# Optimization experiments

Measured on AMD Instinct MI355X. Metric: run time of the kernel, lower is better.

Reference implementation:

```python
import jax, jax.numpy as jnp
import numpy as np

B, S, H = 4, 2048, 1024
NH, HD = 16, 64


def setup_inputs() -> dict:
    key = jax.random.key(0)
    ks = jax.random.split(key, 5)
    scale = 1.0 / np.sqrt(H)
    x = jax.random.normal(ks[0], (B, S, H), dtype=jnp.float32)
    w_qkv = jax.random.normal(ks[1], (H, 3 * H), dtype=jnp.float32) * scale
    b_qkv = jnp.zeros((3 * H,), dtype=jnp.float32)
    w_out = jax.random.normal(ks[2], (H, H), dtype=jnp.float32) * scale
    b_out = jnp.zeros((H,), dtype=jnp.float32)
    return {"x": x, "w_qkv": w_qkv, "b_qkv": b_qkv, "w_out": w_out, "b_out": b_out}


def reference(x, w_qkv, b_qkv, w_out, b_out):
    bsz, seq_len, hidden = x.shape
    qkv = x @ w_qkv + b_qkv  # [B,S,3H]
    q, k, v = jnp.split(qkv, 3, axis=-1)

    def heads(t):
        return t.reshape(bsz, seq_len, NH, HD).transpose(0, 2, 1, 3)  # [B,NH,S,HD]

    q, k, v = heads(q), heads(k), heads(v)
    scale = HD ** (-0.5)
    attn = jnp.einsum("bhqd,bhkd->bhqk", q, k) * scale  # [B,NH,S,S]
    causal = jnp.tril(jnp.ones((seq_len, seq_len), dtype=bool))
    attn = jnp.where(causal, attn, -jnp.inf)
    probs = jax.nn.softmax(attn, axis=-1)
    out = jnp.einsum("bhqk,bhkd->bhqd", probs, v)
    out = out.transpose(0, 2, 1, 3).reshape(bsz, seq_len, hidden)
    return out @ w_out + b_out
```

## Files before the change

kernel.cpp:

```cpp
#include <hip/hip_runtime.h>
#include <hip/hip_bf16.h>
#include <cstdint>

#define B_  4
#define S_  2048
#define H_  1024
#define NH_ 16
#define HD_ 64

using short8  = __attribute__((ext_vector_type(8))) short;
using floatx4 = __attribute__((ext_vector_type(4))) float;

__device__ __forceinline__ unsigned short f2b(float f) {
  union { float f; unsigned int u; } x; x.f = f;
  unsigned int r = x.u + 0x7fffu + ((x.u >> 16) & 1u);
  return (unsigned short)(r >> 16);
}
__device__ __forceinline__ unsigned short f2b_fast(float f) {
  union { float f; unsigned int u; } x; x.f = f;
  return (unsigned short)((x.u + 0x8000u) >> 16);
}
__device__ __forceinline__ unsigned int pack2(float a, float b) {
  return (unsigned int)f2b(a) | ((unsigned int)f2b(b) << 16);
}

__device__ __forceinline__ void async16(void* lds, const void* g) {
  __builtin_amdgcn_global_load_lds(
      (const __attribute__((address_space(1))) unsigned int*)g,
      (__attribute__((address_space(3))) unsigned int*)lds, 16, 0, 0);
}

__global__ void k_convert(const float* __restrict__ in, unsigned short* __restrict__ out, int n) {
  int i = (blockIdx.x * blockDim.x + threadIdx.x) * 4;
  if (i >= n) return;
  float4 v = *(const float4*)(in + i);
  ushort4 o;
  o.x = f2b(v.x); o.y = f2b(v.y); o.z = f2b(v.z); o.w = f2b(v.w);
  *(ushort4*)(out + i) = o;
}

__global__ void k_transpose_convert(const float* __restrict__ in, unsigned short* __restrict__ out,
                                    int R, int C) {
  __shared__ float tile[32][33];
  int tx = threadIdx.x & 31, ty = threadIdx.x >> 5;
  int c0 = blockIdx.x * 32, r0 = blockIdx.y * 32;
  for (int i = 0; i < 4; i++) {
    int r = r0 + ty + i * 8;
    tile[ty + i * 8][tx] = in[(size_t)r * C + c0 + tx];
  }
  __syncthreads();
  for (int i = 0; i < 4; i++) {
    int c = c0 + ty + i * 8;
    out[(size_t)c * R + r0 + tx] = f2b(tile[tx][ty + i * 8]);
  }
}

template <bool OUT_BF16>
__global__ __launch_bounds__(256, 3) void k_gemm_bt(
    const unsigned short* __restrict__ A,
    const unsigned short* __restrict__ BT,
    const float* __restrict__ bias,
    void* __restrict__ Cout,
    unsigned short* __restrict__ vt,
    int M, int N, int K) {
  __shared__ __align__(16) unsigned short As[2][128 * 32];
  __shared__ __align__(16) unsigned short Bs[2][128 * 32];
  const int tid  = threadIdx.x;
  const int lane = tid & 63, wave = tid >> 6;
  const int quad = lane >> 4, l16 = lane & 15;
  const int wm = wave >> 1, wn = wave & 1;
  const int m0 = blockIdx.y * 128, n0 = blockIdx.x * 128;
  const int wv2 = wave & 1;

  const unsigned short* srcbase = (wave < 2) ? A : BT;
  const int base0 = (wave < 2) ? m0 : n0;

  floatx4 acc[4][4];
  for (int mt = 0; mt < 4; mt++)
    for (int nt = 0; nt < 4; nt++)
      acc[mt][nt] = (floatx4){0.f, 0.f, 0.f, 0.f};

  auto stage = [&](int k0, int bufi) {
    unsigned short* dst = (wave < 2) ? &As[bufi][0] : &Bs[bufi][0];
    for (int j = 0; j < 4; j++) {
      int c = wv2 * 256 + j * 64 + lane;
      int row = c >> 2, slot = c & 3;
      int c8 = slot ^ ((row >> 1) & 3);
      async16(&dst[c * 8], &srcbase[(size_t)(base0 + row) * K + k0 + c8 * 8]);
    }
  };

  stage(0, 0);
  int it = 0;
  for (int k0 = 0; k0 < K; k0 += 32, it++) {
    const int cur = it & 1;
    __syncthreads();
    if (k0 + 32 < K) stage(k0 + 32, cur ^ 1);
    short8 af[4], bq[4];
    for (int t = 0; t < 4; t++) {
      int ra = wm * 64 + t * 16 + l16;
      int rb = wn * 64 + t * 16 + l16;
      af[t] = *(const short8*)&As[cur][(ra * 4 + (quad ^ ((ra >> 1) & 3))) * 8];
      bq[t] = *(const short8*)&Bs[cur][(rb * 4 + (quad ^ ((rb >> 1) & 3))) * 8];
    }
    for (int mt = 0; mt < 4; mt++)
      for (int nt = 0; nt < 4; nt++)
        acc[mt][nt] = __builtin_amdgcn_mfma_f32_16x16x32_bf16(af[mt], bq[nt], acc[mt][nt], 0, 0, 0);
  }

  if (OUT_BF16 && n0 >= 2048) {
    for (int mt = 0; mt < 4; mt++) {
      int row0 = m0 + wm * 64 + mt * 16 + quad * 4;
      int b = row0 >> 11, s = row0 & 2047;
      for (int nt = 0; nt < 4; nt++) {
        int col = n0 + wn * 64 + nt * 16 + l16;
        float bv = bias[col];
        uint2 u;
        u.x = pack2(acc[mt][nt][0] + bv, acc[mt][nt][1] + bv);
        u.y = pack2(acc[mt][nt][2] + bv, acc[mt][nt][3] + bv);
        *(uint2*)&vt[(size_t)(b * 1024 + (col - 2048)) * S_ + s] = u;
      }
    }
  } else {
    for (int mt = 0; mt < 4; mt++) {
      int row = m0 + wm * 64 + mt * 16 + quad * 4;
      for (int nt = 0; nt < 4; nt++) {
        int col = n0 + wn * 64 + nt * 16 + l16;
        float bv = bias[col];
        for (int r = 0; r < 4; r++) {
          float v = acc[mt][nt][r] + bv;
          if (OUT_BF16) ((unsigned short*)Cout)[(size_t)(row + r) * N + col] = f2b(v);
          else          ((float*)Cout)[(size_t)(row + r) * N + col] = v;
        }
      }
    }
  }
}

__global__ __launch_bounds__(256, 3) void k_attn(
    const unsigned short* __restrict__ qkv,
    const unsigned short* __restrict__ vt,
    unsigned short* __restrict__ outb) {
  __shared__ __align__(16) unsigned short Ks [2][64 * 64];
  __shared__ __align__(16) unsigned short VTs[2][64 * 64];
  __shared__ __align__(16) unsigned short Ps[4][2][16 * 64];

  const int tid  = threadIdx.x;
  const int lane = tid & 63, w = tid >> 6;
  const int quad = lane >> 4, l16 = lane & 15;
  const int qt = (S_ / 128 - 1) - (blockIdx.x >> 6);
  const int bh = blockIdx.x & 63;
  const int b = bh >> 4, h = bh & 15;
  const int qwv = qt * 128 + w * 32;
  const int wv2 = w & 1;

  short8 qf[2][2];
  for (int g = 0; g < 2; g++)
    for (int kh = 0; kh < 2; kh++)
      qf[g][kh] = *(const short8*)&qkv[(size_t)(b * S_ + qwv + g * 16 + l16) * (3 * H_)
                                       + h * HD_ + kh * 32 + quad * 8];

  floatx4 oacc[2][4];
  float lsum[2] = {0.f, 0.f};
  for (int g = 0; g < 2; g++)
    for (int ct = 0; ct < 4; ct++) oacc[g][ct] = (floatx4){0.f, 0.f, 0.f, 0.f};

  auto stage = [&](int kt, int bufi) {
    if (w < 2) {
      for (int j = 0; j < 4; j++) {
        int c = wv2 * 256 + j * 64 + lane;
        int row = c >> 3, c8 = (c & 7) ^ (row & 7);
        async16(&Ks[bufi][c * 8],
                &qkv[(size_t)(b * S_ + kt * 64 + row) * (3 * H_) + H_ + h * HD_ + c8 * 8]);
      }
    } else {
      for (int j = 0; j < 4; j++) {
        int c = wv2 * 256 + j * 64 + lane;
        int row = c >> 3, c8 = (c & 7) ^ (row & 7);
        async16(&VTs[bufi][c * 8],
                &vt[(size_t)(bh * HD_ + row) * S_ + kt * 64 + c8 * 8]);
      }
    }
  };

  const int ktmax = 2 * qt + 1;
  stage(0, 0);
  for (int kt = 0; kt <= ktmax; kt++) {
    const int cur = kt & 1;
    __syncthreads();
    if (kt < ktmax) stage(kt + 1, cur ^ 1);

    if (kt * 64 <= qwv + 31) {
      const bool need_mask = (kt * 64 + 63 > qwv);

      for (int ct = 0; ct < 4; ct++) {
        int krow = ct * 16 + l16;
        short8 kf0 = *(const short8*)&Ks[cur][(krow * 8 + ((0 + quad) ^ (krow & 7))) * 8];
        short8 kf1 = *(const short8*)&Ks[cur][(krow * 8 + ((4 + quad) ^ (krow & 7))) * 8];
        int slot = (ct * 2 + (quad >> 1)) ^ (l16 & 7);
        for (int g = 0; g < 2; g++) {
          floatx4 z = (floatx4){0.f, 0.f, 0.f, 0.f};
          z = __builtin_amdgcn_mfma_f32_16x16x32_bf16(kf0, qf[g][0], z, 0, 0, 0);
          z = __builtin_amdgcn_mfma_f32_16x16x32_bf16(kf1, qf[g][1], z, 0, 0, 0);
          float p[4];
          if (need_mask) {
            int kvb = kt * 64 + ct * 16 + quad * 4;
            int q = qwv + g * 16 + l16;
            for (int r = 0; r < 4; r++)
              p[r] = (kvb + r <= q) ? __expf(z[r] * 0.125f) : 0.f;
          } else {
            for (int r = 0; r < 4; r++) p[r] = __expf(z[r] * 0.125f);
          }
          lsum[g] += (p[0] + p[1]) + (p[2] + p[3]);
          uint2 u;
          u.x = (unsigned int)f2b_fast(p[0]) | ((unsigned int)f2b_fast(p[1]) << 16);
          u.y = (unsigned int)f2b_fast(p[2]) | ((unsigned int)f2b_fast(p[3]) << 16);
          *(uint2*)&Ps[w][g][l16 * 64 + slot * 8 + (quad & 1) * 4] = u;
        }
      }

      short8 vf[4][2];
      for (int ct = 0; ct < 4; ct++)
        for (int kh = 0; kh < 2; kh++) {
          int vrow = ct * 16 + l16;
          vf[ct][kh] = *(const short8*)&VTs[cur][(vrow * 8 + ((kh * 4 + quad) ^ (vrow & 7))) * 8];
        }

      for (int g = 0; g < 2; g++)
        for (int kh = 0; kh < 2; kh++) {
          short8 pf = *(const short8*)&Ps[w][g][l16 * 64 + ((kh * 4 + quad) ^ (l16 & 7)) * 8];
          for (int ct = 0; ct < 4; ct++)
            oacc[g][ct] = __builtin_amdgcn_mfma_f32_16x16x32_bf16(vf[ct][kh], pf, oacc[g][ct], 0, 0, 0);
        }
    }
  }

  for (int g = 0; g < 2; g++) {
    lsum[g] += __shfl_xor(lsum[g], 16);
    lsum[g] += __shfl_xor(lsum[g], 32);
  }

  for (int g = 0; g < 2; g++) {
    float inv = 1.0f / lsum[g];
    int q = qwv + g * 16 + l16;
    for (int ct = 0; ct < 4; ct++) {
      uint2 u;
      u.x = pack2(oacc[g][ct][0] * inv, oacc[g][ct][1] * inv);
      u.y = pack2(oacc[g][ct][2] * inv, oacc[g][ct][3] * inv);
      *(uint2*)&outb[(size_t)(b * S_ + q) * H_ + h * HD_ + ct * 16 + quad * 4] = u;
    }
  }
}

extern "C" void kernel_launch(void* const* d_in, const int* in_sizes, int n_in,
                              void* d_out, int out_size, void* d_ws, size_t ws_size,
                              hipStream_t stream) {
  const float* x     = (const float*)d_in[0];
  const float* w_qkv = (const float*)d_in[1];
  const float* b_qkv = (const float*)d_in[2];
  const float* w_out = (const float*)d_in[3];
  const float* b_out = (const float*)d_in[4];

  char* ws = (char*)d_ws;
  size_t off = 0;
  auto alloc = [&](size_t bytes) -> void* {
    void* p = ws + off;
    off = (off + bytes + 255) & ~(size_t)255;
    return p;
  };
  unsigned short* xb    = (unsigned short*)alloc((size_t)B_ * S_ * H_ * 2);
  unsigned short* wqkvT = (unsigned short*)alloc((size_t)3 * H_ * H_ * 2);
  unsigned short* woutT = (unsigned short*)alloc((size_t)H_ * H_ * 2);
  unsigned short* qkv   = (unsigned short*)alloc((size_t)B_ * S_ * 3 * H_ * 2);
  unsigned short* ao    = (unsigned short*)alloc((size_t)B_ * S_ * H_ * 2);
  unsigned short* vtb   = (unsigned short*)alloc((size_t)B_ * NH_ * HD_ * S_ * 2);

  const int nx = B_ * S_ * H_;
  k_convert<<<nx / 4 / 256, 256, 0, stream>>>(x, xb, nx);
  k_transpose_convert<<<dim3(3 * H_ / 32, H_ / 32), 256, 0, stream>>>(w_qkv, wqkvT, H_, 3 * H_);
  k_transpose_convert<<<dim3(H_ / 32, H_ / 32), 256, 0, stream>>>(w_out, woutT, H_, H_);

  k_gemm_bt<true ><<<dim3(3 * H_ / 128, B_ * S_ / 128), 256, 0, stream>>>(
      xb, wqkvT, b_qkv, qkv, vtb, B_ * S_, 3 * H_, H_);

  k_attn<<<(S_ / 128) * 64, 256, 0, stream>>>(qkv, vtb, ao);

  k_gemm_bt<false><<<dim3(H_ / 128, B_ * S_ / 128), 256, 0, stream>>>(
      ao, woutT, b_out, (float*)d_out, nullptr, B_ * S_, H_, H_);
}
```

Measured before the change: 250.9 us.

## Enlarge attention query tile to 256 rows and fuse prep kernels

The attention kernel now processes 256 query rows per block (64 per wave, four 16-row groups), so each K/V tile staged into LDS is reused across twice as many queries. The grid becomes 512 blocks with a paired ordering of query tiles meant to balance causal work, and per-group skip checks avoid fully masked tiles. Launch bounds drop to 2 blocks/CU to fit the larger accumulators. The three input conversion and transpose kernels are merged into one launch to cut launch overhead. The cost is more register pressure, lower occupancy and fewer blocks to spread across CUs.

```diff
diff --git a/kernel.cpp b/kernel.cpp
--- a/kernel.cpp
+++ b/kernel.cpp
@@ -30,20 +30,11 @@
       (__attribute__((address_space(3))) unsigned int*)lds, 16, 0, 0);
 }
 
-__global__ void k_convert(const float* __restrict__ in, unsigned short* __restrict__ out, int n) {
-  int i = (blockIdx.x * blockDim.x + threadIdx.x) * 4;
-  if (i >= n) return;
-  float4 v = *(const float4*)(in + i);
-  ushort4 o;
-  o.x = f2b(v.x); o.y = f2b(v.y); o.z = f2b(v.z); o.w = f2b(v.w);
-  *(ushort4*)(out + i) = o;
-}
-
-__global__ void k_transpose_convert(const float* __restrict__ in, unsigned short* __restrict__ out,
-                                    int R, int C) {
+__device__ __forceinline__ void transpose_tile(const float* __restrict__ in,
+                                               unsigned short* __restrict__ out,
+                                               int R, int C, int c0, int r0) {
   __shared__ float tile[32][33];
   int tx = threadIdx.x & 31, ty = threadIdx.x >> 5;
-  int c0 = blockIdx.x * 32, r0 = blockIdx.y * 32;
   for (int i = 0; i < 4; i++) {
     int r = r0 + ty + i * 8;
     tile[ty + i * 8][tx] = in[(size_t)r * C + c0 + tx];
@@ -52,6 +43,26 @@
   for (int i = 0; i < 4; i++) {
     int c = c0 + ty + i * 8;
     out[(size_t)c * R + r0 + tx] = f2b(tile[tx][ty + i * 8]);
+  }
+}
+
+__global__ void k_prep(const float* __restrict__ x, const float* __restrict__ w_qkv,
+                       const float* __restrict__ w_out,
+                       unsigned short* __restrict__ xb, unsigned short* __restrict__ wqkvT,
+                       unsigned short* __restrict__ woutT) {
+  int bx = blockIdx.x;
+  if (bx < 8192) {
+    int i = (bx * 256 + threadIdx.x) * 4;
+    float4 v = *(const float4*)(x + i);
+    ushort4 o;
+    o.x = f2b(v.x); o.y = f2b(v.y); o.z = f2b(v.z); o.w = f2b(v.w);
+    *(ushort4*)(xb + i) = o;
+  } else if (bx < 8192 + 3072) {
+    int t = bx - 8192;
+    transpose_tile(w_qkv, wqkvT, H_, 3 * H_, (t % 96) * 32, (t / 96) * 32);
+  } else {
+    int t = bx - 8192 - 3072;
+    transpose_tile(w_out, woutT, H_, H_, (t & 31) * 32, (t >> 5) * 32);
   }
 }
 
@@ -137,7 +148,7 @@
   }
 }
 
-__global__ __launch_bounds__(256, 3) void k_attn(
+__global__ __launch_bounds__(256, 2) void k_attn(
     const unsigned short* __restrict__ qkv,
     const unsigned short* __restrict__ vt,
     unsigned short* __restrict__ outb) {
@@ -148,21 +159,22 @@
   const int tid  = threadIdx.x;
   const int lane = tid & 63, w = tid >> 6;
   const int quad = lane >> 4, l16 = lane & 15;
-  const int qt = (S_ / 128 - 1) - (blockIdx.x >> 6);
-  const int bh = blockIdx.x & 63;
+  const int bx = blockIdx.x;
+  const int qt = (bx < 256) ? 7 - (bx >> 6) : (bx >> 6) - 4;
+  const int bh = bx & 63;
   const int b = bh >> 4, h = bh & 15;
-  const int qwv = qt * 128 + w * 32;
+  const int qwv = qt * 256 + w * 64;
   const int wv2 = w & 1;
 
-  short8 qf[2][2];
-  for (int g = 0; g < 2; g++)
+  short8 qf[4][2];
+  for (int g = 0; g < 4; g++)
     for (int kh = 0; kh < 2; kh++)
       qf[g][kh] = *(const short8*)&qkv[(size_t)(b * S_ + qwv + g * 16 + l16) * (3 * H_)
                                        + h * HD_ + kh * 32 + quad * 8];
 
-  floatx4 oacc[2][4];
-  float lsum[2] = {0.f, 0.f};
-  for (int g = 0; g < 2; g++)
+  floatx4 oacc[4][4];
+  float lsum[4] = {0.f, 0.f, 0.f, 0.f};
+  for (int g = 0; g < 4; g++)
     for (int ct = 0; ct < 4; ct++) oacc[g][ct] = (floatx4){0.f, 0.f, 0.f, 0.f};
 
   auto stage = [&](int kt, int bufi) {
@@ -183,41 +195,15 @@
     }
   };
 
-  const int ktmax = 2 * qt + 1;
+  const int ktmax = 4 * qt + 3;
   stage(0, 0);
   for (int kt = 0; kt <= ktmax; kt++) {
     const int cur = kt & 1;
     __syncthreads();
     if (kt < ktmax) stage(kt + 1, cur ^ 1);
 
-    if (kt * 64 <= qwv + 31) {
+    if (kt * 64 <= qwv + 63) {
       const bool need_mask = (kt * 64 + 63 > qwv);
-
-      for (int ct = 0; ct < 4; ct++) {
-        int krow = ct * 16 + l16;
-        short8 kf0 = *(const short8*)&Ks[cur][(krow * 8 + ((0 + quad) ^ (krow & 7))) * 8];
-        short8 kf1 = *(const short8*)&Ks[cur][(krow * 8 + ((4 + quad) ^ (krow & 7))) * 8];
-        int slot = (ct * 2 + (quad >> 1)) ^ (l16 & 7);
-        for (int g = 0; g < 2; g++) {
-          floatx4 z = (floatx4){0.f, 0.f, 0.f, 0.f};
-          z = __builtin_amdgcn_mfma_f32_16x16x32_bf16(kf0, qf[g][0], z, 0, 0, 0);
-          z = __builtin_amdgcn_mfma_f32_16x16x32_bf16(kf1, qf[g][1], z, 0, 0, 0);
-          float p[4];
-          if (need_mask) {
-            int kvb = kt * 64 + ct * 16 + quad * 4;
-            int q = qwv + g * 16 + l16;
-            for (int r = 0; r < 4; r++)
-              p[r] = (kvb + r <= q) ? __expf(z[r] * 0.125f) : 0.f;
-          } else {
-            for (int r = 0; r < 4; r++) p[r] = __expf(z[r] * 0.125f);
-          }
-          lsum[g] += (p[0] + p[1]) + (p[2] + p[3]);
-          uint2 u;
-          u.x = (unsigned int)f2b_fast(p[0]) | ((unsigned int)f2b_fast(p[1]) << 16);
-          u.y = (unsigned int)f2b_fast(p[2]) | ((unsigned int)f2b_fast(p[3]) << 16);
-          *(uint2*)&Ps[w][g][l16 * 64 + slot * 8 + (quad & 1) * 4] = u;
-        }
-      }
 
       short8 vf[4][2];
       for (int ct = 0; ct < 4; ct++)
@@ -226,21 +212,57 @@
           vf[ct][kh] = *(const short8*)&VTs[cur][(vrow * 8 + ((kh * 4 + quad) ^ (vrow & 7))) * 8];
         }
 
-      for (int g = 0; g < 2; g++)
-        for (int kh = 0; kh < 2; kh++) {
-          short8 pf = *(const short8*)&Ps[w][g][l16 * 64 + ((kh * 4 + quad) ^ (l16 & 7)) * 8];
-          for (int ct = 0; ct < 4; ct++)
-            oacc[g][ct] = __builtin_amdgcn_mfma_f32_16x16x32_bf16(vf[ct][kh], pf, oacc[g][ct], 0, 0, 0);
+      for (int gp = 0; gp < 2; gp++) {
+        const int g0 = gp * 2;
+        if (kt * 64 > qwv + (g0 + 1) * 16 + 15) continue;
+
+        for (int ct = 0; ct < 4; ct++) {
+          int krow = ct * 16 + l16;
+          short8 kf0 = *(const short8*)&Ks[cur][(krow * 8 + ((0 + quad) ^ (krow & 7))) * 8];
+          short8 kf1 = *(const short8*)&Ks[cur][(krow * 8 + ((4 + quad) ^ (krow & 7))) * 8];
+          int slot = (ct * 2 + (quad >> 1)) ^ (l16 & 7);
+          for (int gi = 0; gi < 2; gi++) {
+            int g = g0 + gi;
+            if (kt * 64 > qwv + g * 16 + 15) continue;
+            floatx4 z = (floatx4){0.f, 0.f, 0.f, 0.f};
+            z = __builtin_amdgcn_mfma_f32_16x16x32_bf16(kf0, qf[g][0], z, 0, 0, 0);
+            z = __builtin_amdgcn_mfma_f32_16x16x32_bf16(kf1, qf[g][1], z, 0, 0, 0);
+            float p[4];
+            if (need_mask) {
+              int kvb = kt * 64 + ct * 16 + quad * 4;
+              int q = qwv + g * 16 + l16;
+              for (int r = 0; r < 4; r++)
+                p[r] = (kvb + r <= q) ? __expf(z[r] * 0.125f) : 0.f;
+            } else {
+              for (int r = 0; r < 4; r++) p[r] = __expf(z[r] * 0.125f);
+            }
+            lsum[g] += (p[0] + p[1]) + (p[2] + p[3]);
+            uint2 u;
+            u.x = (unsigned int)f2b_fast(p[0]) | ((unsigned int)f2b_fast(p[1]) << 16);
+            u.y = (unsigned int)f2b_fast(p[2]) | ((unsigned int)f2b_fast(p[3]) << 16);
+            *(uint2*)&Ps[w][gi][l16 * 64 + slot * 8 + (quad & 1) * 4] = u;
+          }
         }
-    }
-  }
-
-  for (int g = 0; g < 2; g++) {
+
+        for (int gi = 0; gi < 2; gi++) {
+          int g = g0 + gi;
+          if (kt * 64 > qwv + g * 16 + 15) continue;
+          for (int kh = 0; kh < 2; kh++) {
+            short8 pf = *(const short8*)&Ps[w][gi][l16 * 64 + ((kh * 4 + quad) ^ (l16 & 7)) * 8];
+            for (int ct = 0; ct < 4; ct++)
+              oacc[g][ct] = __builtin_amdgcn_mfma_f32_16x16x32_bf16(vf[ct][kh], pf, oacc[g][ct], 0, 0, 0);
+          }
+        }
+      }
+    }
+  }
+
+  for (int g = 0; g < 4; g++) {
     lsum[g] += __shfl_xor(lsum[g], 16);
     lsum[g] += __shfl_xor(lsum[g], 32);
   }
 
-  for (int g = 0; g < 2; g++) {
+  for (int g = 0; g < 4; g++) {
     float inv = 1.0f / lsum[g];
     int q = qwv + g * 16 + l16;
     for (int ct = 0; ct < 4; ct++) {
@@ -275,15 +297,12 @@
   unsigned short* ao    = (unsigned short*)alloc((size_t)B_ * S_ * H_ * 2);
   unsigned short* vtb   = (unsigned short*)alloc((size_t)B_ * NH_ * HD_ * S_ * 2);
 
-  const int nx = B_ * S_ * H_;
-  k_convert<<<nx / 4 / 256, 256, 0, stream>>>(x, xb, nx);
-  k_transpose_convert<<<dim3(3 * H_ / 32, H_ / 32), 256, 0, stream>>>(w_qkv, wqkvT, H_, 3 * H_);
-  k_transpose_convert<<<dim3(H_ / 32, H_ / 32), 256, 0, stream>>>(w_out, woutT, H_, H_);
+  k_prep<<<8192 + 3072 + 1024, 256, 0, stream>>>(x, w_qkv, w_out, xb, wqkvT, woutT);
 
   k_gemm_bt<true ><<<dim3(3 * H_ / 128, B_ * S_ / 128), 256, 0, stream>>>(
       xb, wqkvT, b_qkv, qkv, vtb, B_ * S_, 3 * H_, H_);
 
-  k_attn<<<(S_ / 128) * 64, 256, 0, stream>>>(qkv, vtb, ao);
+  k_attn<<<512, 256, 0, stream>>>(qkv, vtb, ao);
 
   k_gemm_bt<false><<<dim3(H_ / 128, B_ * S_ / 128), 256, 0, stream>>>(
       ao, woutT, b_out, (float*)d_out, nullptr, B_ * S_, H_, H_);
```

After: 286.9 us. 14.4% more time.
